# Optimization experiments

Measured on AMD Instinct MI355X. Metric: run time of the kernel, lower is better.

## Reference

```python
import jax, jax.numpy as jnp
import numpy as np

N_QUBITS = 18
BATCH = 8
LAYERS = 4


def setup_inputs() -> dict:
    key = jax.random.key(0)
    k1, k2 = jax.random.split(key)
    batch_betas = jax.random.normal(k1, (BATCH, LAYERS), dtype=jnp.float32)
    adj_matrices = jax.random.uniform(k2, (BATCH, N_QUBITS, N_QUBITS), dtype=jnp.float32)
    return {"batch_betas": batch_betas, "adj_matrices": adj_matrices}


def reference(batch_betas, adj_matrices):
    B, P = batch_betas.shape
    N = adj_matrices.shape[-1]
    dim = 2 ** N

    # Z_i diagonal for qubit i: ones(2^i) kron [1,-1] kron ones(2^(N-1-i)),
    # i.e. z_i(x) = 1 - 2 * bit_{N-1-i}(x).
    idx = jnp.arange(dim)
    shifts = (N - 1 - jnp.arange(N))[:, None]
    Z = 1.0 - 2.0 * ((idx[None, :] >> shifts) & 1).astype(jnp.float32)  # [N, dim]

    # MaxCut diagonal: sum over upper-triangular edges of 0.5 * (1 - z_u * z_v)
    W = (jnp.triu(adj_matrices, k=1) > 0.5).astype(jnp.float32)  # [B, N, N]
    n_edges = jnp.sum(W, axis=(1, 2))                            # [B]
    T = jnp.einsum('buv,vd->bud', W, Z)                          # [B, N, dim]
    cross = jnp.einsum('bud,ud->bd', T, Z)                       # sum_{u<v} W z_u z_v
    hp_diag = 0.5 * (n_edges[:, None] - cross)                   # [B, dim]

    # uniform superposition
    state = jnp.full((B, dim), 1.0 / np.sqrt(dim), dtype=jnp.complex64)
    phase = jnp.exp(-1j * hp_diag)  # e^{-i * H_P * 1.0}, complex64

    for t in range(P):
        state = state * phase
        beta = batch_betas[:, t]
        c = jnp.cos(beta).astype(jnp.complex64)[:, None, None]
        ms = (-1j * jnp.sin(beta).astype(jnp.complex64))[:, None, None]
        # apply RX-like mixer [[c, -i s], [-i s, c]] to each qubit
        for i in range(N):
            s4 = state.reshape(B, 2 ** i, 2, -1)
            s0 = s4[:, :, 0, :]
            s1 = s4[:, :, 1, :]
            new0 = c * s0 + ms * s1
            new1 = ms * s0 + c * s1
            state = jnp.stack([new0, new1], axis=2).reshape(B, dim)

    probs = jnp.abs(state) ** 2
    energy = jnp.sum(probs * hp_diag, axis=1)  # [B]
    return energy
```

## Files before the change

kernel.cpp:

```cpp
#include <hip/hip_runtime.h>
#include <hip/hip_fp16.h>

#define NQ 18
#define QDIM (1 << NQ)
#define NB 8
#define NL 4

typedef unsigned u32;
typedef unsigned long long u64;

#define DPP_XOR1 0xB1
#define DPP_XOR2 0x4E

__device__ __forceinline__ void tbfly(float2& a, float2& b, float t) {
  float nax = fmaf(t, b.y, a.x);
  float nay = fmaf(-t, b.x, a.y);
  float nbx = fmaf(t, a.y, b.x);
  float nby = fmaf(-t, a.x, b.y);
  a = make_float2(nax, nay); b = make_float2(nbx, nby);
}
__device__ __forceinline__ void tstage8(float2* v, int m, float t) {
#pragma unroll
  for (int i = 0; i < 8; ++i)
    if (!(i & m)) tbfly(v[i], v[i | m], t);
}
template <int CTRL>
__device__ __forceinline__ void dppstage8(float2* v, float t) {
#pragma unroll
  for (int k = 0; k < 8; ++k) {
    float ox = __int_as_float(
        __builtin_amdgcn_mov_dpp(__float_as_int(v[k].x), CTRL, 0xF, 0xF, true));
    float oy = __int_as_float(
        __builtin_amdgcn_mov_dpp(__float_as_int(v[k].y), CTRL, 0xF, 0xF, true));
    v[k] = make_float2(fmaf(t, oy, v[k].x), fmaf(-t, ox, v[k].y));
  }
}
__device__ __forceinline__ void shfl32stage8(float2* v, float t) {
#pragma unroll
  for (int k = 0; k < 8; ++k) {
    float ox = __shfl_xor(v[k].x, 32, 64);
    float oy = __shfl_xor(v[k].y, 32, 64);
    v[k] = make_float2(fmaf(t, oy, v[k].x), fmaf(-t, ox, v[k].y));
  }
}
__device__ __forceinline__ void mix6(float2* v, float t) {
  tstage8(v, 1, t); tstage8(v, 2, t); tstage8(v, 4, t);
  dppstage8<DPP_XOR1>(v, t); dppstage8<DPP_XOR2>(v, t);
  shfl32stage8(v, t);
}
__device__ __forceinline__ void pmul(float2& a, float2 p) {
  a = make_float2(a.x * p.x - a.y * p.y, a.x * p.y + a.y * p.x);
}
__device__ __forceinline__ int swz(int byte) { return byte ^ (((byte >> 7) & 7) << 4); }

__device__ __forceinline__ float2 h2f(u32 u) {
  __half2 h; *(u32*)&h = u; return __half22float2(h);
}
__device__ __forceinline__ u32 f2h(float2 f) {
  __half2 h = __float22half2_rn(f); return *(u32*)&h;
}

template <int MODE>
__global__ __launch_bounds__(512)
void k_low(const float* __restrict__ betas, const float* __restrict__ adj,
           unsigned char* __restrict__ hp8, u32* __restrict__ state,
           float* __restrict__ out, int t0) {
  __shared__ float2 swapb[4096];
  __shared__ float2 ptab[160];
  __shared__ unsigned smask[NQ];
  __shared__ unsigned sfull[3];
  __shared__ int sdeg[3];
  __shared__ float wsum[8];

  const int tid = threadIdx.x;
  const int l = tid & 63, w = tid >> 6;
  const int b = blockIdx.x & 7;
  const int blk6 = blockIdx.x >> 3;
  const size_t bb = (size_t)b << NQ;
  const int lbase = blk6 << 12;
  char* L = (char*)swapb;
  const int constB = ((w >> 2) << 8) | (((l >> 5) & 1) << 7) | (((l >> 1) & 1) << 6)
                   | ((l & 1) << 5) | ((w & 3) << 3) | ((l >> 2) & 7);
  const int bBbase = constB << 3;

  const float beta0 = betas[b * NL + t0];
  float s0, c0; sincosf(beta0, &s0, &c0);
  const float tf0 = s0 / c0;
  const float c0p2 = c0 * c0, c0p4 = c0p2 * c0p2;
  const float c0p12 = c0p4 * c0p4 * c0p4;

  float tf1 = 0.f, scale = 1.f;
  if (MODE == 0) scale = 0.001953125f * c0p12;
  if (MODE == 1) {
    const float beta1 = betas[b * NL + t0 + 1];
    float s1, c1; sincosf(beta1, &s1, &c1);
    tf1 = s1 / c1;
    const float c1p2 = c1 * c1, c1p4 = c1p2 * c1p2;
    scale = c0p12 * (c1p4 * c1p4 * c1p4);
  }

  if (MODE == 0) {
    if (tid < NQ) {
      unsigned m = 0;
      const float* row = adj + ((size_t)b * NQ + tid) * NQ;
      for (int vq = tid + 1; vq < NQ; ++vq)
        if (row[vq] > 0.5f) m |= 1u << (NQ - 1 - vq);
      smask[tid] = m;
    }
    if (blk6 == 0 && tid == 0) out[b] = 0.f;
    if (tid < 160) {
      float ss, cc; sincosf((float)tid, &ss, &cc);
      ptab[tid] = make_float2(cc * scale, -ss * scale);
    }
    __syncthreads();
    if (tid < 3) {
      unsigned fm = smask[17 - tid];
      for (int uq = 0; uq < NQ; ++uq)
        if ((smask[uq] >> tid) & 1u) fm |= 1u << (17 - uq);
      sfull[tid] = fm; sdeg[tid] = __popc(fm);
    }
    __syncthreads();
  } else if (MODE == 1) {
    if (tid < 160) {
      float ss, cc; sincosf((float)tid, &ss, &cc);
      ptab[tid] = make_float2(cc * scale, -ss * scale);
    }
    __syncthreads();
  }

  float2 v[8];

  if (MODE == 0) {
    unsigned d = (unsigned)(lbase | (tid << 3));
    int hp = 0;
#pragma unroll
    for (int uq = 0; uq < NQ; ++uq) {
      const unsigned f = (d >> (17 - uq)) & 1u;
      hp += __popc(smask[uq] & (d ^ (0u - f)));
    }
    u64 pk = (u64)hp;
    int j = 0;
#pragma unroll
    for (int i = 1; i < 8; ++i) {
      const int p = __ffs(i) - 1;
      const int old = (int)((d >> p) & 1u);
      const int nb1 = __popc(sfull[p] & d);
      hp += old ? (2 * nb1 - sdeg[p]) : (sdeg[p] - 2 * nb1);
      d ^= 1u << p; j ^= 1 << p;
      pk |= (u64)hp << (8 * j);
    }
    *(u64*)(hp8 + bb + (size_t)(lbase + (tid << 3))) = pk;
#pragma unroll
    for (int jj = 0; jj < 8; ++jj)
      v[jj] = ptab[(int)((pk >> (8 * jj)) & 255)];
    mix6(v, tf0);
#pragma unroll
    for (int q = 0; q < 4; ++q)
      *(float4*)(L + swz((tid << 6) | (q << 4))) =
          make_float4(v[2*q].x, v[2*q].y, v[2*q+1].x, v[2*q+1].y);
    __syncthreads();
#pragma unroll
    for (int jj = 0; jj < 8; ++jj)
      v[jj] = *(const float2*)(L + swz((jj << 12) + bBbase));
    mix6(v, tf0);
#pragma unroll
    for (int jj = 0; jj < 8; ++jj)
      *(float2*)(L + swz((jj << 12) + bBbase)) = v[jj];
    __syncthreads();
#pragma unroll
    for (int q = 0; q < 4; ++q) {
      const float4 f = *(const float4*)(L + swz((tid << 6) | (q << 4)));
      v[2*q]   = make_float2(f.x, f.y);
      v[2*q+1] = make_float2(f.z, f.w);
    }
    uint4* gdst = (uint4*)(state + bb + lbase + (tid << 3));
    gdst[0] = make_uint4(f2h(v[0]), f2h(v[1]), f2h(v[2]), f2h(v[3]));
    gdst[1] = make_uint4(f2h(v[4]), f2h(v[5]), f2h(v[6]), f2h(v[7]));
    return;
  }

  const uint4* gsrc = (const uint4*)(state + bb + lbase + (tid << 3));
  {
    const uint4 t4a = gsrc[0], t4b = gsrc[1];
    v[0] = h2f(t4a.x); v[1] = h2f(t4a.y); v[2] = h2f(t4a.z); v[3] = h2f(t4a.w);
    v[4] = h2f(t4b.x); v[5] = h2f(t4b.y); v[6] = h2f(t4b.z); v[7] = h2f(t4b.w);
  }
  mix6(v, tf0);
#pragma unroll
  for (int q = 0; q < 4; ++q)
    *(float4*)(L + swz((tid << 6) | (q << 4))) =
        make_float4(v[2*q].x, v[2*q].y, v[2*q+1].x, v[2*q+1].y);
  __syncthreads();
#pragma unroll
  for (int jj = 0; jj < 8; ++jj)
    v[jj] = *(const float2*)(L + swz((jj << 12) + bBbase));
  mix6(v, tf0);

  if (MODE == 1) {
    const unsigned char* hq = hp8 + bb + (size_t)(lbase + constB);
#pragma unroll
    for (int jj = 0; jj < 8; ++jj)
      pmul(v[jj], ptab[hq[jj << 9]]);
    mix6(v, tf1);
#pragma unroll
    for (int jj = 0; jj < 8; ++jj)
      *(float2*)(L + swz((jj << 12) + bBbase)) = v[jj];
    __syncthreads();
#pragma unroll
    for (int q = 0; q < 4; ++q) {
      const float4 f = *(const float4*)(L + swz((tid << 6) | (q << 4)));
      v[2*q]   = make_float2(f.x, f.y);
      v[2*q+1] = make_float2(f.z, f.w);
    }
    mix6(v, tf1);
    uint4* gdst = (uint4*)(state + bb + lbase + (tid << 3));
    gdst[0] = make_uint4(f2h(v[0]), f2h(v[1]), f2h(v[2]), f2h(v[3]));
    gdst[1] = make_uint4(f2h(v[4]), f2h(v[5]), f2h(v[6]), f2h(v[7]));
  } else {
    const unsigned char* hq = hp8 + bb + (size_t)(lbase + constB);
    float acc = 0.f;
#pragma unroll
    for (int jj = 0; jj < 8; ++jj) {
      const float h = (float)hq[jj << 9];
      const float wx = v[jj].x * c0p12, wy = v[jj].y * c0p12;
      acc = fmaf(wx * wx + wy * wy, h, acc);
    }
#pragma unroll
    for (int m = 1; m <= 32; m <<= 1) acc += __shfl_xor(acc, m, 64);
    if (l == 0) wsum[w] = acc;
    __syncthreads();
    if (tid == 0) {
      float s = 0.f;
#pragma unroll
      for (int i = 0; i < 8; ++i) s += wsum[i];
      atomicAdd(out + b, s);
    }
  }
}

__global__ __launch_bounds__(512)
void k_high(const float* __restrict__ betas, const unsigned char* __restrict__ hp8,
            u32* __restrict__ state, int t0) {
  __shared__ float2 swapb[4096];
  __shared__ float2 ptab[160];
  const int tid = threadIdx.x;
  const int col = tid & 63, w = tid >> 6;
  const int b = blockIdx.x & 7;
  const int mid = blockIdx.x >> 3;
  const size_t bb = (size_t)b << NQ;
  const int cbase = (mid << 6) | col;

  const float beta0 = betas[b * NL + t0], beta1 = betas[b * NL + t0 + 1];
  float s0, c0, s1, c1;
  sincosf(beta0, &s0, &c0); sincosf(beta1, &s1, &c1);
  const float tf0 = s0 / c0, tf1 = s1 / c1;
  const float c0p2 = c0 * c0, c1p2 = c1 * c1;
  const float scale = (c0p2 * c0p2 * c0p2) * (c1p2 * c1p2 * c1p2);
  if (tid < 160) {
    float ss, cc; sincosf((float)tid, &ss, &cc);
    ptab[tid] = make_float2(cc * scale, -ss * scale);
  }
  __syncthreads();

  float2 v[8];
#pragma unroll
  for (int j = 0; j < 8; ++j)
    v[j] = h2f(state[bb + ((size_t)((w << 3) | j) << 12) + cbase]);
  tstage8(v, 1, tf0); tstage8(v, 2, tf0); tstage8(v, 4, tf0);
#pragma unroll
  for (int j = 0; j < 8; ++j)
    swapb[(((w << 3) | j) << 6) | col] = v[j];
  __syncthreads();
#pragma unroll
  for (int j = 0; j < 8; ++j)
    v[j] = swapb[(((j << 3) | w) << 6) | col];
  tstage8(v, 1, tf0); tstage8(v, 2, tf0); tstage8(v, 4, tf0);
#pragma unroll
  for (int j = 0; j < 8; ++j) {
    const int h = hp8[bb + ((size_t)((j << 3) | w) << 12) + cbase];
    pmul(v[j], ptab[h]);
  }
  tstage8(v, 1, tf1); tstage8(v, 2, tf1); tstage8(v, 4, tf1);
#pragma unroll
  for (int j = 0; j < 8; ++j)
    swapb[(((j << 3) | w) << 6) | col] = v[j];
  __syncthreads();
#pragma unroll
  for (int j = 0; j < 8; ++j)
    v[j] = swapb[(((w << 3) | j) << 6) | col];
  tstage8(v, 1, tf1); tstage8(v, 2, tf1); tstage8(v, 4, tf1);
#pragma unroll
  for (int j = 0; j < 8; ++j)
    state[bb + ((size_t)((w << 3) | j) << 12) + cbase] = f2h(v[j]);
}

extern "C" void kernel_launch(void* const* d_in, const int* in_sizes, int n_in,
                              void* d_out, int out_size, void* d_ws, size_t ws_size,
                              hipStream_t stream) {
  const float* betas = (const float*)d_in[0];
  const float* adj   = (const float*)d_in[1];
  float* out = (float*)d_out;
  char* ws = (char*)d_ws;
  u32* state = (u32*)ws;
  unsigned char* hp8 = (unsigned char*)(ws + (size_t)NB * QDIM * 4);

  dim3 grid(NB * 64), blk(512);
  k_low<0><<<grid, blk, 0, stream>>>(betas, adj, hp8, state, out, 0);
  k_high  <<<grid, blk, 0, stream>>>(betas, hp8, state, 0);
  k_low<1><<<grid, blk, 0, stream>>>(betas, adj, hp8, state, out, 1);
  k_high  <<<grid, blk, 0, stream>>>(betas, hp8, state, 2);
  k_low<2><<<grid, blk, 0, stream>>>(betas, adj, hp8, state, out, 3);
}
```

Before: 41.42 us.

## Fuse five phase kernels into one persistent kernel with per-batch grid barriers

Replaces the five separate kernel launches with one persistent kernel of 256 blocks. Each block handles two tiles per phase, and phases are separated by per-batch atomic counter barriers over 32 blocks. A small init kernel zeroes the barrier counters and the output. State loads become relaxed agent-scope atomics so that data written by other blocks is seen across the barriers. This removes launch gaps and kernel boundaries, but it depends on all 256 blocks being co-resident, halves the parallelism per phase, and adds spin-wait overhead; the barrier spin has a guard that breaks out after a bounded number of iterations.

```diff
diff --git a/kernel.cpp b/kernel.cpp
--- a/kernel.cpp
+++ b/kernel.cpp
@@ -60,73 +60,49 @@
   __half2 h = __float22half2_rn(f); return *(u32*)&h;
 }
 
+__device__ __forceinline__ void ld_state8(const u32* p, float2* v) {
+  u64* q = (u64*)p;
+#pragma unroll
+  for (int i = 0; i < 4; ++i) {
+    const u64 wv = __hip_atomic_load(q + i, __ATOMIC_RELAXED, __HIP_MEMORY_SCOPE_AGENT);
+    v[2*i]   = h2f((u32)wv);
+    v[2*i+1] = h2f((u32)(wv >> 32));
+  }
+}
+__device__ __forceinline__ float2 ld_state1(const u32* p) {
+  return h2f(__hip_atomic_load((u32*)p, __ATOMIC_RELAXED, __HIP_MEMORY_SCOPE_AGENT));
+}
+
+__device__ __forceinline__ void batchbar(u32* cnt) {
+  asm volatile("s_waitcnt vmcnt(0) lgkmcnt(0)" ::: "memory");
+  __syncthreads();
+  if (threadIdx.x == 0) {
+    __hip_atomic_fetch_add(cnt, 1u, __ATOMIC_RELAXED, __HIP_MEMORY_SCOPE_AGENT);
+    int guard = 0;
+    while (__hip_atomic_load(cnt, __ATOMIC_RELAXED, __HIP_MEMORY_SCOPE_AGENT) < 32u) {
+      __builtin_amdgcn_s_sleep(2);
+      if (++guard > (1 << 21)) break;
+    }
+  }
+  __syncthreads();
+}
+
 template <int MODE>
-__global__ __launch_bounds__(512)
-void k_low(const float* __restrict__ betas, const float* __restrict__ adj,
-           unsigned char* __restrict__ hp8, u32* __restrict__ state,
-           float* __restrict__ out, int t0) {
-  __shared__ float2 swapb[4096];
-  __shared__ float2 ptab[160];
-  __shared__ unsigned smask[NQ];
-  __shared__ unsigned sfull[3];
-  __shared__ int sdeg[3];
-  __shared__ float wsum[8];
-
-  const int tid = threadIdx.x;
+__device__ __forceinline__
+void low_body(const int tid, const int b, const int blk6,
+              const float tf0, const float tf1, const float escale,
+              float2* __restrict__ swapb, const float2* __restrict__ ptab,
+              const unsigned* __restrict__ smask, const unsigned* __restrict__ sfull,
+              const int* __restrict__ sdeg, float* __restrict__ wsum,
+              unsigned char* __restrict__ hp8, u32* __restrict__ state,
+              float* __restrict__ out) {
   const int l = tid & 63, w = tid >> 6;
-  const int b = blockIdx.x & 7;
-  const int blk6 = blockIdx.x >> 3;
   const size_t bb = (size_t)b << NQ;
   const int lbase = blk6 << 12;
   char* L = (char*)swapb;
   const int constB = ((w >> 2) << 8) | (((l >> 5) & 1) << 7) | (((l >> 1) & 1) << 6)
                    | ((l & 1) << 5) | ((w & 3) << 3) | ((l >> 2) & 7);
   const int bBbase = constB << 3;
-
-  const float beta0 = betas[b * NL + t0];
-  float s0, c0; sincosf(beta0, &s0, &c0);
-  const float tf0 = s0 / c0;
-  const float c0p2 = c0 * c0, c0p4 = c0p2 * c0p2;
-  const float c0p12 = c0p4 * c0p4 * c0p4;
-
-  float tf1 = 0.f, scale = 1.f;
-  if (MODE == 0) scale = 0.001953125f * c0p12;
-  if (MODE == 1) {
-    const float beta1 = betas[b * NL + t0 + 1];
-    float s1, c1; sincosf(beta1, &s1, &c1);
-    tf1 = s1 / c1;
-    const float c1p2 = c1 * c1, c1p4 = c1p2 * c1p2;
-    scale = c0p12 * (c1p4 * c1p4 * c1p4);
-  }
-
-  if (MODE == 0) {
-    if (tid < NQ) {
-      unsigned m = 0;
-      const float* row = adj + ((size_t)b * NQ + tid) * NQ;
-      for (int vq = tid + 1; vq < NQ; ++vq)
-        if (row[vq] > 0.5f) m |= 1u << (NQ - 1 - vq);
-      smask[tid] = m;
-    }
-    if (blk6 == 0 && tid == 0) out[b] = 0.f;
-    if (tid < 160) {
-      float ss, cc; sincosf((float)tid, &ss, &cc);
-      ptab[tid] = make_float2(cc * scale, -ss * scale);
-    }
-    __syncthreads();
-    if (tid < 3) {
-      unsigned fm = smask[17 - tid];
-      for (int uq = 0; uq < NQ; ++uq)
-        if ((smask[uq] >> tid) & 1u) fm |= 1u << (17 - uq);
-      sfull[tid] = fm; sdeg[tid] = __popc(fm);
-    }
-    __syncthreads();
-  } else if (MODE == 1) {
-    if (tid < 160) {
-      float ss, cc; sincosf((float)tid, &ss, &cc);
-      ptab[tid] = make_float2(cc * scale, -ss * scale);
-    }
-    __syncthreads();
-  }
 
   float2 v[8];
 
@@ -179,12 +155,7 @@
     return;
   }
 
-  const uint4* gsrc = (const uint4*)(state + bb + lbase + (tid << 3));
-  {
-    const uint4 t4a = gsrc[0], t4b = gsrc[1];
-    v[0] = h2f(t4a.x); v[1] = h2f(t4a.y); v[2] = h2f(t4a.z); v[3] = h2f(t4a.w);
-    v[4] = h2f(t4b.x); v[5] = h2f(t4b.y); v[6] = h2f(t4b.z); v[7] = h2f(t4b.w);
-  }
+  ld_state8(state + bb + lbase + (tid << 3), v);
   mix6(v, tf0);
 #pragma unroll
   for (int q = 0; q < 4; ++q)
@@ -222,7 +193,7 @@
 #pragma unroll
     for (int jj = 0; jj < 8; ++jj) {
       const float h = (float)hq[jj << 9];
-      const float wx = v[jj].x * c0p12, wy = v[jj].y * c0p12;
+      const float wx = v[jj].x * escale, wy = v[jj].y * escale;
       acc = fmaf(wx * wx + wy * wy, h, acc);
     }
 #pragma unroll
@@ -235,37 +206,23 @@
       for (int i = 0; i < 8; ++i) s += wsum[i];
       atomicAdd(out + b, s);
     }
-  }
-}
-
-__global__ __launch_bounds__(512)
-void k_high(const float* __restrict__ betas, const unsigned char* __restrict__ hp8,
-            u32* __restrict__ state, int t0) {
-  __shared__ float2 swapb[4096];
-  __shared__ float2 ptab[160];
-  const int tid = threadIdx.x;
+    __syncthreads();
+  }
+}
+
+__device__ __forceinline__
+void high_body(const int tid, const int b, const int mid,
+               const float tf0, const float tf1,
+               float2* __restrict__ swapb, const float2* __restrict__ ptab,
+               const unsigned char* __restrict__ hp8, u32* __restrict__ state) {
   const int col = tid & 63, w = tid >> 6;
-  const int b = blockIdx.x & 7;
-  const int mid = blockIdx.x >> 3;
   const size_t bb = (size_t)b << NQ;
   const int cbase = (mid << 6) | col;
-
-  const float beta0 = betas[b * NL + t0], beta1 = betas[b * NL + t0 + 1];
-  float s0, c0, s1, c1;
-  sincosf(beta0, &s0, &c0); sincosf(beta1, &s1, &c1);
-  const float tf0 = s0 / c0, tf1 = s1 / c1;
-  const float c0p2 = c0 * c0, c1p2 = c1 * c1;
-  const float scale = (c0p2 * c0p2 * c0p2) * (c1p2 * c1p2 * c1p2);
-  if (tid < 160) {
-    float ss, cc; sincosf((float)tid, &ss, &cc);
-    ptab[tid] = make_float2(cc * scale, -ss * scale);
-  }
-  __syncthreads();
-
   float2 v[8];
-#pragma unroll
-  for (int j = 0; j < 8; ++j)
-    v[j] = h2f(state[bb + ((size_t)((w << 3) | j) << 12) + cbase]);
+
+#pragma unroll
+  for (int j = 0; j < 8; ++j)
+    v[j] = ld_state1(state + bb + ((size_t)((w << 3) | j) << 12) + cbase);
   tstage8(v, 1, tf0); tstage8(v, 2, tf0); tstage8(v, 4, tf0);
 #pragma unroll
   for (int j = 0; j < 8; ++j)
@@ -292,6 +249,122 @@
 #pragma unroll
   for (int j = 0; j < 8; ++j)
     state[bb + ((size_t)((w << 3) | j) << 12) + cbase] = f2h(v[j]);
+}
+
+__global__ void k_init(u32* __restrict__ bar, float* __restrict__ out) {
+  const int t = threadIdx.x;
+  if (t < 128) bar[t] = 0u;
+  if (t >= 128 && t < 128 + NB) out[t - 128] = 0.f;
+}
+
+__global__ __launch_bounds__(512)
+void k_fused(const float* __restrict__ betas, const float* __restrict__ adj,
+             unsigned char* __restrict__ hp8, u32* __restrict__ state,
+             float* __restrict__ out, u32* __restrict__ bar) {
+  __shared__ float2 swapb[4096];
+  __shared__ float2 ptab[160];
+  __shared__ unsigned smask[NQ];
+  __shared__ unsigned sfull[3];
+  __shared__ int sdeg[3];
+  __shared__ float wsum[8];
+
+  const int tid = threadIdx.x;
+  const int b = blockIdx.x & 7;
+  const int idx = blockIdx.x >> 3;
+  u32* mybar = bar + b * 16;
+
+  float tf[4], cp6[4], cp12[4];
+#pragma unroll
+  for (int t = 0; t < 4; ++t) {
+    float s, c; sincosf(betas[b * NL + t], &s, &c);
+    tf[t] = s / c;
+    const float c2 = c * c;
+    cp6[t] = c2 * c2 * c2;
+    cp12[t] = cp6[t] * cp6[t];
+  }
+
+  if (tid < NQ) {
+    unsigned m = 0;
+    const float* row = adj + ((size_t)b * NQ + tid) * NQ;
+    for (int vq = tid + 1; vq < NQ; ++vq)
+      if (row[vq] > 0.5f) m |= 1u << (NQ - 1 - vq);
+    smask[tid] = m;
+  }
+  {
+    const float sc = 0.001953125f * cp12[0];
+    if (tid < 160) {
+      float ss, cc; sincosf((float)tid, &ss, &cc);
+      ptab[tid] = make_float2(cc * sc, -ss * sc);
+    }
+  }
+  __syncthreads();
+  if (tid < 3) {
+    unsigned fm = smask[17 - tid];
+    for (int uq = 0; uq < NQ; ++uq)
+      if ((smask[uq] >> tid) & 1u) fm |= 1u << (17 - uq);
+    sfull[tid] = fm; sdeg[tid] = __popc(fm);
+  }
+  __syncthreads();
+#pragma unroll
+  for (int s = 0; s < 2; ++s) {
+    if (s) __syncthreads();
+    low_body<0>(tid, b, (idx << 1) | s, tf[0], 0.f, 0.f, swapb, ptab, smask,
+                sfull, sdeg, wsum, hp8, state, out);
+  }
+  batchbar(mybar + 0);
+
+  {
+    const float sc = cp6[0] * cp6[1];
+    if (tid < 160) {
+      float ss, cc; sincosf((float)tid, &ss, &cc);
+      ptab[tid] = make_float2(cc * sc, -ss * sc);
+    }
+  }
+  __syncthreads();
+#pragma unroll
+  for (int s = 0; s < 2; ++s) {
+    if (s) __syncthreads();
+    high_body(tid, b, (idx << 1) | s, tf[0], tf[1], swapb, ptab, hp8, state);
+  }
+  batchbar(mybar + 1);
+
+  {
+    const float sc = cp12[1] * cp12[2];
+    if (tid < 160) {
+      float ss, cc; sincosf((float)tid, &ss, &cc);
+      ptab[tid] = make_float2(cc * sc, -ss * sc);
+    }
+  }
+  __syncthreads();
+#pragma unroll
+  for (int s = 0; s < 2; ++s) {
+    if (s) __syncthreads();
+    low_body<1>(tid, b, (idx << 1) | s, tf[1], tf[2], 0.f, swapb, ptab, smask,
+                sfull, sdeg, wsum, hp8, state, out);
+  }
+  batchbar(mybar + 2);
+
+  {
+    const float sc = cp6[2] * cp6[3];
+    if (tid < 160) {
+      float ss, cc; sincosf((float)tid, &ss, &cc);
+      ptab[tid] = make_float2(cc * sc, -ss * sc);
+    }
+  }
+  __syncthreads();
+#pragma unroll
+  for (int s = 0; s < 2; ++s) {
+    if (s) __syncthreads();
+    high_body(tid, b, (idx << 1) | s, tf[2], tf[3], swapb, ptab, hp8, state);
+  }
+  batchbar(mybar + 3);
+
+#pragma unroll
+  for (int s = 0; s < 2; ++s) {
+    if (s) __syncthreads();
+    low_body<2>(tid, b, (idx << 1) | s, tf[3], 0.f, cp12[3], swapb, ptab, smask,
+                sfull, sdeg, wsum, hp8, state, out);
+  }
 }
 
 extern "C" void kernel_launch(void* const* d_in, const int* in_sizes, int n_in,
@@ -303,11 +376,8 @@
   char* ws = (char*)d_ws;
   u32* state = (u32*)ws;
   unsigned char* hp8 = (unsigned char*)(ws + (size_t)NB * QDIM * 4);
-
-  dim3 grid(NB * 64), blk(512);
-  k_low<0><<<grid, blk, 0, stream>>>(betas, adj, hp8, state, out, 0);
-  k_high  <<<grid, blk, 0, stream>>>(betas, hp8, state, 0);
-  k_low<1><<<grid, blk, 0, stream>>>(betas, adj, hp8, state, out, 1);
-  k_high  <<<grid, blk, 0, stream>>>(betas, hp8, state, 2);
-  k_low<2><<<grid, blk, 0, stream>>>(betas, adj, hp8, state, out, 3);
-}
+  u32* bar = (u32*)(ws + (size_t)NB * QDIM * 5);
+
+  k_init<<<1, 192, 0, stream>>>(bar, out);
+  k_fused<<<256, 512, 0, stream>>>(betas, adj, hp8, state, out, bar);
+}
```

New measurement: 45.15 us. 1.09x slower.
